# Kernel tuning notes

Hardware: AMD Instinct MI355X
Metric: run time of the kernel (lower is better)

The kernel has to match this reference:

```python
import jax, jax.numpy as jnp
import numpy as np

E, S, D_IN, D_LAT, D_HID = 1024, 64, 128, 128, 512
NSTEPS, DT = 8192, 0.01
KL_WEIGHT = 0.01


def setup_inputs() -> dict:
    key = jax.random.key(0)
    ks = jax.random.split(key, 12)
    sd = lambda fan_in: 1.0 / np.sqrt(fan_in)
    return {
        'event_marks': jax.random.normal(ks[0], (E, D_IN), jnp.float32),
        'z_events': jax.random.normal(ks[1], (E, S, D_LAT), jnp.float32),
        'z_traj': jax.random.normal(ks[2], (NSTEPS, S, D_LAT), jnp.float32),
        'times': jnp.arange(NSTEPS + 1, dtype=jnp.float32) * DT,
        'Wp': jax.random.normal(ks[3], (D_IN, D_LAT), jnp.float32) * sd(D_IN),
        'bp': jnp.zeros((D_LAT,), jnp.float32),
        'W1': jax.random.normal(ks[4], (D_LAT, D_HID), jnp.float32) * sd(D_LAT),
        'b1': jnp.zeros((D_HID,), jnp.float32),
        'W2': jax.random.normal(ks[5], (D_HID, 1), jnp.float32) * sd(D_HID),
        'b2': jnp.zeros((1,), jnp.float32),
        'base_intensity': jnp.asarray(0.1, jnp.float32),
        'Wd1': jax.random.normal(ks[6], (D_LAT, D_HID), jnp.float32) * sd(D_LAT),
        'bd1': jnp.zeros((D_HID,), jnp.float32),
        'Wd2': jax.random.normal(ks[7], (D_HID, D_LAT), jnp.float32) * sd(D_HID),
        'bd2': jnp.zeros((D_LAT,), jnp.float32),
    }


def reference(event_marks, z_events, z_traj, times, Wp, bp, W1, b1, W2, b2,
              base_intensity, Wd1, bd1, Wd2, bd2):
    # input projection of marks: [E, D_LAT]
    marks_proj = event_marks @ Wp + bp

    def intensity(z):  # z: [..., D_LAT] -> [...]
        h = jax.nn.relu(z @ W1 + b1)
        s = (h @ W2 + b2)[..., 0]
        return jax.nn.softplus(s + base_intensity)

    # log-intensity at events: sum over events of mean over samples
    lam_ev = intensity(z_events)                      # [E, S]
    log_intensity_sum = jnp.log(lam_ev + 1e-8).mean(axis=1).sum()

    # compensator integral over the trajectory (left Riemann sum)
    lam_traj = intensity(z_traj)                      # [NSTEPS, S]
    dts = jnp.diff(times)                             # [NSTEPS]
    integral = (lam_traj.mean(axis=1) * dts).sum()

    # Gaussian decoder log-prob: mu = MLP(z), unit variance
    h = jax.nn.relu(z_events @ Wd1 + bd1)             # [E, S, D_HID]
    mu = h @ Wd2 + bd2                                # [E, S, D_LAT]
    x = marks_proj[:, None, :]                        # [E, 1, D_LAT]
    log_2pi = jnp.log(jnp.asarray(2.0 * np.pi, jnp.float32))
    log_p = -0.5 * jnp.sum((x - mu) ** 2, axis=-1) - 0.5 * D_LAT * log_2pi  # [E, S]
    recon_loss = log_p.mean(axis=1).sum()

    kl_loss = KL_WEIGHT * jnp.mean(z_traj ** 2)

    elbo = log_intensity_sum - integral + recon_loss - kl_loss
    return -elbo
```

## Files before the change

### kernel.cpp

```cpp
#include <hip/hip_runtime.h>

typedef __attribute__((ext_vector_type(4))) float f32x4;
typedef __attribute__((ext_vector_type(8))) __bf16 bf16x8;
typedef __attribute__((ext_vector_type(4))) __bf16 bf16x4;

#define LOG_2PI 1.8378770664093453f

__device__ __forceinline__ float softplus_f(float x) {
  return fmaxf(x, 0.f) + log1pf(expf(-fabsf(x)));
}

__device__ __forceinline__ void barrier_lds_only() {
  asm volatile("s_waitcnt lgkmcnt(0)\n\ts_barrier" ::: "memory");
}

__global__ void prep_kernel(const float* __restrict__ em,
                            const float* __restrict__ Wp,
                            const float* __restrict__ bp,
                            float* __restrict__ mp,
                            float* __restrict__ accs) {
  const int b = blockIdx.x;
  if (b == 1024) {
    if (threadIdx.x < 8) accs[threadIdx.x] = 0.f;
    return;
  }
  const int d = threadIdx.x;
  float s = bp[d];
  const float* emr = em + b * 128;
#pragma unroll 4
  for (int k = 0; k < 128; ++k) s += emr[k] * Wp[k * 128 + d];
  mp[b * 128 + d] = s;
}

__global__ __launch_bounds__(768, 3) void intensity11_kernel(
    const float* __restrict__ z_traj, const float* __restrict__ z_ev,
    const float* __restrict__ W1, const float* __restrict__ b1,
    const float* __restrict__ W2, const float* __restrict__ b2,
    const float* __restrict__ base_i, const float* __restrict__ times,
    float* __restrict__ accs) {
  __shared__ __align__(16) __bf16 w1t[512 * 128];
  __shared__ __align__(16) float b1L[512];
  __shared__ __align__(16) float w2L[512];
  __shared__ float red[12][4];

  const int tid = threadIdx.x;
  const int wid = tid >> 6, lid = tid & 63;
  const int g = lid >> 4, q = lid & 15;
  const int gw = blockIdx.x * 12 + wid;
  const int h0 = gw * 6;

  f32x4 stg[2][4][2];

#define ZROW(H) ((H) < 16384 ? z_traj + (size_t)(H) * 4096 \
                             : z_ev + (size_t)((H) - 16384) * 4096)
#define LOADH(ZP)                                                          \
  do {                                                                     \
    _Pragma("unroll") for (int s = 0; s < 2; ++s) {                        \
      const float* rp = (ZP) + (s * 16 + q) * 128 + g * 8;                 \
      _Pragma("unroll") for (int kf = 0; kf < 4; ++kf) {                   \
        stg[s][kf][0] = *(const f32x4*)(rp + kf * 32);                     \
        stg[s][kf][1] = *(const f32x4*)(rp + kf * 32 + 4);                 \
      }                                                                    \
    }                                                                      \
  } while (0)

  LOADH(ZROW(h0));

  if (tid < 512) {
    const float* wcol = W1 + tid;
    char* wbs = (char*)w1t;
    const int colbase = tid * 256;
    const int sw = (tid & 7) << 4;
#pragma unroll 8
    for (int k = 0; k < 128; k += 2) {
      float a = wcol[(size_t)k * 512];
      float c = wcol[(size_t)(k + 1) * 512];
      union { __bf16 h[2]; unsigned u; } pk;
      pk.h[0] = (__bf16)a;
      pk.h[1] = (__bf16)c;
      *(unsigned*)(wbs + (colbase + ((k * 2) ^ sw))) = pk.u;
    }
    b1L[tid] = b1[tid];
    w2L[tid] = W2[tid];
  }
  const float sbias = b2[0] + base_i[0];
  barrier_lds_only();

  float integral_loc = 0.f, logsum_loc = 0.f, kls = 0.f;
  const char* wb = (const char*)w1t;
  const int wsw = (q & 7) << 4;

#pragma unroll 1
  for (int r = 0; r < 6; ++r) {
    const int h = h0 + r;
    const bool traj_h = (h < 16384);

    bf16x8 fr[2][4];
#pragma unroll
    for (int s = 0; s < 2; ++s) {
#pragma unroll
      for (int kf = 0; kf < 4; ++kf) {
        f32x4 a0 = stg[s][kf][0], a1 = stg[s][kf][1];
        if (traj_h) {
          kls += a0[0] * a0[0] + a0[1] * a0[1] + a0[2] * a0[2] + a0[3] * a0[3];
          kls += a1[0] * a1[0] + a1[1] * a1[1] + a1[2] * a1[2] + a1[3] * a1[3];
        }
        bf16x8 f;
#pragma unroll
        for (int j = 0; j < 4; ++j) {
          f[j] = (__bf16)a0[j];
          f[4 + j] = (__bf16)a1[j];
        }
        fr[s][kf] = f;
      }
    }

    if (r < 5) LOADH(ZROW(h + 1));
    __builtin_amdgcn_sched_barrier(0);

    float rowacc0 = 0.f, rowacc1 = 0.f;
#pragma unroll 4
    for (int c = 0; c < 32; ++c) {
      f32x4 a0 = {}, a1 = {};
#pragma unroll
      for (int kf = 0; kf < 4; ++kf) {
        bf16x8 wf = *(const bf16x8*)(wb + c * 4096 + q * 256 +
                                     ((kf * 64 + g * 16) ^ wsw));
        a0 = __builtin_amdgcn_mfma_f32_16x16x32_bf16(wf, fr[0][kf], a0, 0, 0, 0);
        a1 = __builtin_amdgcn_mfma_f32_16x16x32_bf16(wf, fr[1][kf], a1, 0, 0, 0);
      }
      f32x4 bb = *(const f32x4*)&b1L[c * 16 + g * 4];
      f32x4 ww = *(const f32x4*)&w2L[c * 16 + g * 4];
#pragma unroll
      for (int ii = 0; ii < 4; ++ii) {
        rowacc0 += fmaxf(a0[ii] + bb[ii], 0.f) * ww[ii];
        rowacc1 += fmaxf(a1[ii] + bb[ii], 0.f) * ww[ii];
      }
    }
    rowacc0 += __shfl_xor(rowacc0, 16);
    rowacc0 += __shfl_xor(rowacc0, 32);
    rowacc1 += __shfl_xor(rowacc1, 16);
    rowacc1 += __shfl_xor(rowacc1, 32);

    if (lid < 32) {
      const float rs = (lid < 16) ? rowacc0 : rowacc1;
      const float lam = softplus_f(rs + sbias);
      if (traj_h) {
        const int ts = h >> 1;
        integral_loc += lam * (times[ts + 1] - times[ts]) * (1.f / 64.f);
      } else {
        logsum_loc += logf(lam + 1e-8f) * (1.f / 64.f);
      }
    }
  }
#undef LOADH
#undef ZROW

#pragma unroll
  for (int m = 32; m >= 1; m >>= 1) {
    integral_loc += __shfl_xor(integral_loc, m);
    logsum_loc += __shfl_xor(logsum_loc, m);
    kls += __shfl_xor(kls, m);
  }
  if (lid == 0) {
    red[wid][0] = integral_loc;
    red[wid][1] = logsum_loc;
    red[wid][2] = kls;
  }
  __syncthreads();
  if (tid == 0) {
    float I = 0.f, L = 0.f, K = 0.f;
#pragma unroll
    for (int w = 0; w < 12; ++w) {
      I += red[w][0];
      L += red[w][1];
      K += red[w][2];
    }
    atomicAdd(&accs[0], I);
    atomicAdd(&accs[1], L);
    atomicAdd(&accs[3], K);
  }
}

__global__ __launch_bounds__(512, 2) void decoder2_kernel(
    const float* __restrict__ z,
    const float* __restrict__ Wd1, const float* __restrict__ bd1,
    const float* __restrict__ Wd2, const float* __restrict__ bd2,
    const float* __restrict__ mp, float* __restrict__ recon_acc) {
  __shared__ __align__(16) __bf16 zbuf[2][32 * 128];
  __shared__ __align__(16) __bf16 hbuf[32 * 512];
  __shared__ float s_part[32][9];
  __shared__ float red[8];

  const int tid = threadIdx.x;
  const int wid = tid >> 6, lid = tid & 63;
  const int g = lid >> 4, q = lid & 15;
  const int cb = wid * 64;
  const int tile0 = blockIdx.x * 4;

  bf16x8 bw1[4][4];
  f32x4 bd1v[4];
#pragma unroll
  for (int cf = 0; cf < 4; ++cf) {
    const int col = cb + cf * 16 + q;
#pragma unroll
    for (int i = 0; i < 4; ++i) bd1v[cf][i] = bd1[cb + cf * 16 + g * 4 + i];
#pragma unroll
    for (int kf = 0; kf < 4; ++kf) {
      bf16x8 f;
#pragma unroll
      for (int j = 0; j < 8; ++j) f[j] = (__bf16)Wd1[(kf * 32 + g * 8 + j) * 512 + col];
      bw1[cf][kf] = f;
    }
  }
  const int dimf = wid * 16 + q;
  bf16x8 bw2[16];
#pragma unroll
  for (int kf2 = 0; kf2 < 16; ++kf2) {
    bf16x8 f;
#pragma unroll
    for (int j = 0; j < 8; ++j) f[j] = (__bf16)Wd2[(kf2 * 32 + g * 8 + j) * 128 + dimf];
    bw2[kf2] = f;
  }
  f32x4 bd2v;
#pragma unroll
  for (int i = 0; i < 4; ++i) bd2v[i] = bd2[wid * 16 + g * 4 + i];

  const int srow = tid >> 4, sk8 = (tid & 15) * 8;
  const int stg_byte = ((srow * 256 + sk8 * 2) ^ ((srow & 7) << 4));
  char* hb = (char*)hbuf;

  float local = 0.f;

  {
    const float* p = z + (size_t)tile0 * 4096 + tid * 8;
    f32x4 r0 = *(const f32x4*)p, r1 = *(const f32x4*)(p + 4);
    bf16x8 v;
#pragma unroll
    for (int j = 0; j < 4; ++j) { v[j] = (__bf16)r0[j]; v[4 + j] = (__bf16)r1[j]; }
    *(bf16x8*)((char*)zbuf[0] + stg_byte) = v;
  }
  f32x4 rA0, rA1, rB0, rB1;
  { const float* p = z + (size_t)(tile0 + 1) * 4096 + tid * 8; rA0 = *(const f32x4*)p; rA1 = *(const f32x4*)(p + 4); }
  { const float* p = z + (size_t)(tile0 + 2) * 4096 + tid * 8; rB0 = *(const f32x4*)p; rB1 = *(const f32x4*)(p + 4); }
  barrier_lds_only();

#define DBODY(T, ZC, RR0, RR1)                                                     \
  do {                                                                             \
    f32x4 acc1[2][4] = {};                                                         \
    char* zc = (char*)zbuf[ZC];                                                    \
    _Pragma("unroll") for (int kf = 0; kf < 4; ++kf) {                             \
      _Pragma("unroll") for (int rf = 0; rf < 2; ++rf) {                           \
        const int row = rf * 16 + q;                                               \
        bf16x8 a = *(const bf16x8*)(zc + ((row * 256 + kf * 64 + g * 16) ^ ((row & 7) << 4))); \
        _Pragma("unroll") for (int cf = 0; cf < 4; ++cf)                           \
          acc1[rf][cf] = __builtin_amdgcn_mfma_f32_16x16x32_bf16(bw1[cf][kf], a, acc1[rf][cf], 0, 0, 0); \
      }                                                                            \
    }                                                                              \
    {                                                                              \
      bf16x8 v;                                                                    \
      _Pragma("unroll") for (int j = 0; j < 4; ++j) { v[j] = (__bf16)RR0[j]; v[4 + j] = (__bf16)RR1[j]; } \
      *(bf16x8*)((char*)zbuf[(ZC) ^ 1] + stg_byte) = v;                            \
    }                                                                              \
    {                                                                              \
      int tl = (T) + 3; if (tl > 3) tl = 3;                                        \
      const float* p = z + (size_t)(tile0 + tl) * 4096 + tid * 8;                  \
      RR0 = *(const f32x4*)p; RR1 = *(const f32x4*)(p + 4);                        \
    }                                                                              \
    _Pragma("unroll") for (int rf = 0; rf < 2; ++rf) {                             \
      const int row = rf * 16 + q;                                                 \
      _Pragma("unroll") for (int cf = 0; cf < 4; ++cf) {                           \
        bf16x4 hv;                                                                 \
        _Pragma("unroll") for (int i = 0; i < 4; ++i)                              \
          hv[i] = (__bf16)fmaxf(acc1[rf][cf][i] + bd1v[cf][i], 0.f);               \
        const int byt = ((row * 1024 + (cb + cf * 16 + g * 4) * 2) ^ ((row & 7) << 4)); \
        *(bf16x4*)(hb + byt) = hv;                                                 \
      }                                                                            \
    }                                                                              \
    barrier_lds_only();                                                            \
    f32x4 acc2[2] = {};                                                            \
    _Pragma("unroll") for (int kf2 = 0; kf2 < 16; ++kf2) {                         \
      _Pragma("unroll") for (int rf2 = 0; rf2 < 2; ++rf2) {                        \
        const int row = rf2 * 16 + q;                                              \
        bf16x8 a = *(const bf16x8*)(hb + ((row * 1024 + kf2 * 64 + g * 16) ^ ((row & 7) << 4))); \
        acc2[rf2] = __builtin_amdgcn_mfma_f32_16x16x32_bf16(bw2[kf2], a, acc2[rf2], 0, 0, 0); \
      }                                                                            \
    }                                                                              \
    const int e = (tile0 + (T)) >> 1;                                              \
    _Pragma("unroll") for (int rf2 = 0; rf2 < 2; ++rf2) {                          \
      float partial = 0.f;                                                         \
      _Pragma("unroll") for (int i = 0; i < 4; ++i) {                              \
        const float xv = mp[e * 128 + wid * 16 + g * 4 + i];                       \
        const float d = xv - (acc2[rf2][i] + bd2v[i]);                             \
        partial += d * d;                                                          \
      }                                                                            \
      partial += __shfl_xor(partial, 16);                                          \
      partial += __shfl_xor(partial, 32);                                          \
      if (lid < 16) s_part[rf2 * 16 + lid][wid] = partial;                         \
    }                                                                              \
    barrier_lds_only();                                                            \
    if (tid < 32) {                                                                \
      float t2 = 0.f;                                                              \
      _Pragma("unroll") for (int w = 0; w < 8; ++w) t2 += s_part[tid][w];          \
      local += (-0.5f * t2 - 0.5f * 128.f * LOG_2PI) * (1.f / 64.f);               \
    }                                                                              \
  } while (0)

#pragma unroll 1
  for (int t = 0; t < 4; t += 2) {
    DBODY(t, 0, rA0, rA1);
    DBODY(t + 1, 1, rB0, rB1);
  }
#undef DBODY

  if (wid == 0) {
#pragma unroll
    for (int m = 16; m >= 1; m >>= 1) local += __shfl_xor(local, m);
    if (lid == 0) atomicAdd(recon_acc, local);
  }
}

__global__ void finalize_kernel(const float* __restrict__ accs, float* __restrict__ out) {
  const float kl = 0.01f * (accs[3] / 67108864.f);
  const float elbo = accs[1] - accs[0] + accs[2] - kl;
  out[0] = -elbo;
}

extern "C" void kernel_launch(void* const* d_in, const int* in_sizes, int n_in,
                              void* d_out, int out_size, void* d_ws, size_t ws_size,
                              hipStream_t stream) {
  const float* event_marks = (const float*)d_in[0];
  const float* z_events = (const float*)d_in[1];
  const float* z_traj = (const float*)d_in[2];
  const float* times = (const float*)d_in[3];
  const float* Wp = (const float*)d_in[4];
  const float* bp = (const float*)d_in[5];
  const float* W1 = (const float*)d_in[6];
  const float* b1 = (const float*)d_in[7];
  const float* W2 = (const float*)d_in[8];
  const float* b2 = (const float*)d_in[9];
  const float* base_i = (const float*)d_in[10];
  const float* Wd1 = (const float*)d_in[11];
  const float* bd1 = (const float*)d_in[12];
  const float* Wd2 = (const float*)d_in[13];
  const float* bd2 = (const float*)d_in[14];

  float* mp = (float*)d_ws;
  float* accs = (float*)((char*)d_ws + 1024 * 128 * 4);

  prep_kernel<<<1025, 128, 0, stream>>>(event_marks, Wp, bp, mp, accs);
  intensity11_kernel<<<256, 768, 0, stream>>>(z_traj, z_events, W1, b1, W2, b2,
                                              base_i, times, accs);
  decoder2_kernel<<<512, 512, 0, stream>>>(z_events, Wd1, bd1, Wd2, bd2, mp,
                                           &accs[2]);
  finalize_kernel<<<1, 1, 0, stream>>>(accs, (float*)d_out);
}
```

Baseline: 156.2 us.

## Fold mark projection into intensity kernel, rebalance warps, halve decoder tiles

```diff
diff --git a/kernel.cpp b/kernel.cpp
--- a/kernel.cpp
+++ b/kernel.cpp
@@ -14,40 +14,37 @@
   asm volatile("s_waitcnt lgkmcnt(0)\n\ts_barrier" ::: "memory");
 }
 
-__global__ void prep_kernel(const float* __restrict__ em,
-                            const float* __restrict__ Wp,
-                            const float* __restrict__ bp,
-                            float* __restrict__ mp,
-                            float* __restrict__ accs) {
-  const int b = blockIdx.x;
-  if (b == 1024) {
-    if (threadIdx.x < 8) accs[threadIdx.x] = 0.f;
-    return;
-  }
-  const int d = threadIdx.x;
-  float s = bp[d];
-  const float* emr = em + b * 128;
-#pragma unroll 4
-  for (int k = 0; k < 128; ++k) s += emr[k] * Wp[k * 128 + d];
-  mp[b * 128 + d] = s;
-}
-
-__global__ __launch_bounds__(768, 3) void intensity11_kernel(
+__global__ __launch_bounds__(1024, 1) void intensity12_kernel(
     const float* __restrict__ z_traj, const float* __restrict__ z_ev,
     const float* __restrict__ W1, const float* __restrict__ b1,
     const float* __restrict__ W2, const float* __restrict__ b2,
     const float* __restrict__ base_i, const float* __restrict__ times,
+    const float* __restrict__ em, const float* __restrict__ Wp,
+    const float* __restrict__ bp, float* __restrict__ mp,
     float* __restrict__ accs) {
   __shared__ __align__(16) __bf16 w1t[512 * 128];
   __shared__ __align__(16) float b1L[512];
   __shared__ __align__(16) float w2L[512];
-  __shared__ float red[12][4];
+  __shared__ float red[16][4];
 
   const int tid = threadIdx.x;
+
+  if (blockIdx.x >= 256) {
+    const int e = (blockIdx.x - 256) * 8 + (tid >> 7);
+    const int d = tid & 127;
+    float s = bp[d];
+    const float* emr = em + e * 128;
+#pragma unroll 4
+    for (int k = 0; k < 128; ++k) s += emr[k] * Wp[k * 128 + d];
+    mp[e * 128 + d] = s;
+    return;
+  }
+
   const int wid = tid >> 6, lid = tid & 63;
   const int g = lid >> 4, q = lid & 15;
-  const int gw = blockIdx.x * 12 + wid;
-  const int h0 = gw * 6;
+  const int gw = blockIdx.x * 16 + wid;
+  const int nh = (gw < 2048) ? 5 : 4;
+  const int h0 = (gw < 2048) ? gw * 5 : 10240 + (gw - 2048) * 4;
 
   f32x4 stg[2][4][2];
 
@@ -91,7 +88,7 @@
   const int wsw = (q & 7) << 4;
 
 #pragma unroll 1
-  for (int r = 0; r < 6; ++r) {
+  for (int r = 0; r < nh; ++r) {
     const int h = h0 + r;
     const bool traj_h = (h < 16384);
 
@@ -115,7 +112,7 @@
       }
     }
 
-    if (r < 5) LOADH(ZROW(h + 1));
+    if (r + 1 < nh) LOADH(ZROW(h + 1));
     __builtin_amdgcn_sched_barrier(0);
 
     float rowacc0 = 0.f, rowacc1 = 0.f;
@@ -171,7 +168,7 @@
   if (tid == 0) {
     float I = 0.f, L = 0.f, K = 0.f;
 #pragma unroll
-    for (int w = 0; w < 12; ++w) {
+    for (int w = 0; w < 16; ++w) {
       I += red[w][0];
       L += red[w][1];
       K += red[w][2];
@@ -182,7 +179,7 @@
   }
 }
 
-__global__ __launch_bounds__(512, 2) void decoder2_kernel(
+__global__ __launch_bounds__(512, 2) void decoder3_kernel(
     const float* __restrict__ z,
     const float* __restrict__ Wd1, const float* __restrict__ bd1,
     const float* __restrict__ Wd2, const float* __restrict__ bd2,
@@ -196,7 +193,7 @@
   const int wid = tid >> 6, lid = tid & 63;
   const int g = lid >> 4, q = lid & 15;
   const int cb = wid * 64;
-  const int tile0 = blockIdx.x * 4;
+  const int tile0 = blockIdx.x * 2;
 
   bf16x8 bw1[4][4];
   f32x4 bd1v[4];
@@ -240,15 +237,18 @@
     for (int j = 0; j < 4; ++j) { v[j] = (__bf16)r0[j]; v[4 + j] = (__bf16)r1[j]; }
     *(bf16x8*)((char*)zbuf[0] + stg_byte) = v;
   }
-  f32x4 rA0, rA1, rB0, rB1;
-  { const float* p = z + (size_t)(tile0 + 1) * 4096 + tid * 8; rA0 = *(const f32x4*)p; rA1 = *(const f32x4*)(p + 4); }
-  { const float* p = z + (size_t)(tile0 + 2) * 4096 + tid * 8; rB0 = *(const f32x4*)p; rB1 = *(const f32x4*)(p + 4); }
+  f32x4 rA0, rA1;
+  {
+    const float* p = z + (size_t)(tile0 + 1) * 4096 + tid * 8;
+    rA0 = *(const f32x4*)p;
+    rA1 = *(const f32x4*)(p + 4);
+  }
   barrier_lds_only();
 
-#define DBODY(T, ZC, RR0, RR1)                                                     \
+#define DBODY(T, DO_STAGE)                                                         \
   do {                                                                             \
     f32x4 acc1[2][4] = {};                                                         \
-    char* zc = (char*)zbuf[ZC];                                                    \
+    char* zc = (char*)zbuf[(T)];                                                   \
     _Pragma("unroll") for (int kf = 0; kf < 4; ++kf) {                             \
       _Pragma("unroll") for (int rf = 0; rf < 2; ++rf) {                           \
         const int row = rf * 16 + q;                                               \
@@ -257,15 +257,10 @@
           acc1[rf][cf] = __builtin_amdgcn_mfma_f32_16x16x32_bf16(bw1[cf][kf], a, acc1[rf][cf], 0, 0, 0); \
       }                                                                            \
     }                                                                              \
-    {                                                                              \
+    if (DO_STAGE) {                                                                \
       bf16x8 v;                                                                    \
-      _Pragma("unroll") for (int j = 0; j < 4; ++j) { v[j] = (__bf16)RR0[j]; v[4 + j] = (__bf16)RR1[j]; } \
-      *(bf16x8*)((char*)zbuf[(ZC) ^ 1] + stg_byte) = v;                            \
-    }                                                                              \
-    {                                                                              \
-      int tl = (T) + 3; if (tl > 3) tl = 3;                                        \
-      const float* p = z + (size_t)(tile0 + tl) * 4096 + tid * 8;                  \
-      RR0 = *(const f32x4*)p; RR1 = *(const f32x4*)(p + 4);                        \
+      _Pragma("unroll") for (int j = 0; j < 4; ++j) { v[j] = (__bf16)rA0[j]; v[4 + j] = (__bf16)rA1[j]; } \
+      *(bf16x8*)((char*)zbuf[1] + stg_byte) = v;                                   \
     }                                                                              \
     _Pragma("unroll") for (int rf = 0; rf < 2; ++rf) {                             \
       const int row = rf * 16 + q;                                                 \
@@ -304,13 +299,11 @@
       _Pragma("unroll") for (int w = 0; w < 8; ++w) t2 += s_part[tid][w];          \
       local += (-0.5f * t2 - 0.5f * 128.f * LOG_2PI) * (1.f / 64.f);               \
     }                                                                              \
+    barrier_lds_only();                                                            \
   } while (0)
 
-#pragma unroll 1
-  for (int t = 0; t < 4; t += 2) {
-    DBODY(t, 0, rA0, rA1);
-    DBODY(t + 1, 1, rB0, rB1);
-  }
+  DBODY(0, true);
+  DBODY(1, false);
 #undef DBODY
 
   if (wid == 0) {
@@ -348,10 +341,11 @@
   float* mp = (float*)d_ws;
   float* accs = (float*)((char*)d_ws + 1024 * 128 * 4);
 
-  prep_kernel<<<1025, 128, 0, stream>>>(event_marks, Wp, bp, mp, accs);
-  intensity11_kernel<<<256, 768, 0, stream>>>(z_traj, z_events, W1, b1, W2, b2,
-                                              base_i, times, accs);
-  decoder2_kernel<<<512, 512, 0, stream>>>(z_events, Wd1, bd1, Wd2, bd2, mp,
-                                           &accs[2]);
+  (void)hipMemsetAsync(accs, 0, 4 * sizeof(float), stream);
+  intensity12_kernel<<<384, 1024, 0, stream>>>(z_traj, z_events, W1, b1, W2, b2,
+                                               base_i, times, event_marks, Wp,
+                                               bp, mp, accs);
+  decoder3_kernel<<<1024, 512, 0, stream>>>(z_events, Wd1, bd1, Wd2, bd2, mp,
+                                            &accs[2]);
   finalize_kernel<<<1, 1, 0, stream>>>(accs, (float*)d_out);
 }
```

After: 192.6 us. +23.3%, slower.
